# Kernel tuning notes

Measured on AMD Instinct MI355X. Metric: run time of the kernel, lower is better.

## Reference

```python
import jax, jax.numpy as jnp
import numpy as np

E = 128   # embedding_dim
H = 4     # num_heads
D = E * H # internal width = 512 (MHA head_dim = E)
B = 512
N = 128


def setup_inputs() -> dict:
    key = jax.random.key(0)
    ks = jax.random.split(key, 16)
    s = lambda fan_in: 1.0 / np.sqrt(fan_in)
    u = lambda k, shape, sc: jax.random.uniform(k, shape, jnp.float32, -sc, sc)
    inp = {
        "x": jax.random.normal(ks[0], (B, N, E), jnp.float32),
        "weights": jax.random.uniform(ks[1], (B, N, 1), jnp.float32),
        # self.embedding: Linear(E, D)
        "emb_W": u(ks[2], (D, E), s(E)), "emb_b": u(ks[3], (D,), s(E)),
        # outer W_q/W_k/W_v: Linear(D, D)
        "wq_W": u(ks[4], (D, D), s(D)), "wq_b": u(ks[5], (D,), s(D)),
        "wk_W": u(ks[6], (D, D), s(D)), "wk_b": u(ks[7], (D,), s(D)),
        "wv_W": u(ks[8], (D, D), s(D)), "wv_b": u(ks[9], (D,), s(D)),
        # nn.MultiheadAttention packed in-projection (out_proj is irrelevant:
        # its output is discarded, only att_weights are used)
        "in_proj_W": u(ks[10], (3 * D, D), s(D)),
        "in_proj_b": jnp.zeros((3 * D,), jnp.float32),
        # LayerNorm(D)
        "ln_g": jnp.ones((D,), jnp.float32), "ln_b": jnp.zeros((D,), jnp.float32),
        # self.out: Linear(D, E)
        "out_W": u(ks[11], (E, D), s(D)), "out_b": u(ks[12], (E,), s(D)),
    }
    return inp


def reference(x, weights, emb_W, emb_b, wq_W, wq_b, wk_W, wk_b, wv_W, wv_b,
              in_proj_W, in_proj_b, ln_g, ln_b, out_W, out_b):
    # x: [B, N, E] -> embedded [B, N, D]
    xe = x @ emb_W.T + emb_b
    # key_padding_mask: rows of xe that are all-zero
    pad = jnp.sum(jnp.abs(xe), axis=-1) == 0.0              # [B, N] bool

    # outer projections
    q_in = xe @ wq_W.T + wq_b
    k_in = xe @ wk_W.T + wk_b
    v_in = xe @ wv_W.T + wv_b                               # [B, N, D]

    # MHA internal packed in-projection
    Wq, Wk, Wv = in_proj_W[:D], in_proj_W[D:2 * D], in_proj_W[2 * D:]
    bq, bk, bv = in_proj_b[:D], in_proj_b[D:2 * D], in_proj_b[2 * D:]
    hd = D // H  # head_dim = E
    to_heads = lambda t: t.reshape(t.shape[0], t.shape[1], H, hd).transpose(0, 2, 1, 3)
    q = to_heads(q_in @ Wq.T + bq)                          # [B, H, N, hd]
    k = to_heads(k_in @ Wk.T + bk)

    scores = jnp.einsum('bhie,bhje->bhij', q, k) / jnp.sqrt(jnp.float32(hd))
    scores = jnp.where(pad[:, None, None, :], -jnp.inf, scores)
    attn = jax.nn.softmax(scores, axis=-1)                  # [B, H, N, N]
    att_weights = jnp.mean(attn, axis=1)                    # averaged over heads [B, N, N]

    # external reweighting + renormalization
    att_weights = att_weights * jnp.swapaxes(weights, -2, -1)  # [B,N,N]*[B,1,N]
    att_weights = att_weights / jnp.sum(att_weights, axis=-1, keepdims=True)

    # re-apply to outer V projection (MHA's own output is discarded)
    att_output = jnp.einsum('bij,bjd->bid', att_weights, v_in)

    h = xe + jax.nn.softplus(att_output)
    mu = jnp.mean(h, axis=-1, keepdims=True)
    var = jnp.mean((h - mu) ** 2, axis=-1, keepdims=True)
    h = (h - mu) / jnp.sqrt(var + 1e-5) * ln_g + ln_b
    return h @ out_W.T + out_b                              # [B, N, E]
```

## Files before the change

### kernel.cpp

```cpp
#include <hip/hip_runtime.h>
#include <stdint.h>


typedef __attribute__((ext_vector_type(8))) __bf16 bf16x8;
typedef __attribute__((ext_vector_type(8))) uint16_t u16x8;
typedef __attribute__((ext_vector_type(4))) float f32x4;

__device__ __forceinline__ float b2f(uint16_t h) {
  union { uint32_t u; float f; } c; c.u = ((uint32_t)h) << 16; return c.f;
}
__device__ __forceinline__ uint16_t f2b(float f) {
  union { float f; uint32_t u; } c; c.f = f;
  return (uint16_t)((c.u + 0x7fffu + ((c.u >> 16) & 1u)) >> 16);
}
__device__ __forceinline__ void gld16(void* lds, const void* g) {
  __builtin_amdgcn_global_load_lds(
      (const __attribute__((address_space(1))) uint32_t*)(g),
      (__attribute__((address_space(3))) uint32_t*)(lds),
      16, 0, 0);
}

#define MFMA16(a, b, c) __builtin_amdgcn_mfma_f32_16x16x32_bf16((a), (b), (c), 0, 0, 0)

__global__ __launch_bounds__(256) void pack_bf16(const float* __restrict__ in,
                                                 uint16_t* __restrict__ out, int n4) {
  int i = blockIdx.x * 256 + threadIdx.x;
  if (i >= n4) return;
  float4 v = ((const float4*)in)[i];
  ushort4 o;
  o.x = f2b(v.x); o.y = f2b(v.y); o.z = f2b(v.z); o.w = f2b(v.w);
  ((ushort4*)out)[i] = o;
}

__global__ __launch_bounds__(256) void pack_w6(
    const float* __restrict__ emb_W, const float* __restrict__ wq_W,
    const float* __restrict__ wk_W, const float* __restrict__ wv_W,
    const float* __restrict__ ipW, const float* __restrict__ out_W,
    uint16_t* __restrict__ embW2, uint16_t* __restrict__ wqW_bf,
    uint16_t* __restrict__ wkW_bf, uint16_t* __restrict__ Wvc,
    uint16_t* __restrict__ ip_bf, uint16_t* __restrict__ owW_bf) {
  int i = blockIdx.x * 256 + threadIdx.x;
  const float* src; uint16_t* dst; int off;
  if (i < 16384)       { src = emb_W; dst = embW2;  off = i; }
  else if (i < 81920)  { src = wq_W;  dst = wqW_bf; off = i - 16384; }
  else if (i < 147456) { src = wk_W;  dst = wkW_bf; off = i - 81920; }
  else if (i < 212992) { src = wv_W;  dst = Wvc;    off = i - 147456; }
  else if (i < 344064) { src = ipW;   dst = ip_bf;  off = i - 212992; }
  else if (i < 360448) { src = out_W; dst = owW_bf; off = i - 344064; }
  else return;
  float4 v = ((const float4*)src)[off];
  ushort4 o;
  o.x = f2b(v.x); o.y = f2b(v.y); o.z = f2b(v.z); o.w = f2b(v.w);
  ((ushort4*)dst)[off] = o;
}

__global__ __launch_bounds__(256) void bias_stage1(
    const float* __restrict__ wq_W, const float* __restrict__ wk_W,
    const float* __restrict__ wv_W, const float* __restrict__ emb_b,
    const float* __restrict__ wq_b, const float* __restrict__ wk_b,
    const float* __restrict__ wv_b,
    float* __restrict__ t1q, float* __restrict__ t1k, float* __restrict__ bve,
    float* __restrict__ pad_init, float* __restrict__ biasE) {
  const int gid = blockIdx.x * 256 + threadIdx.x;
  if (gid < 65536) pad_init[gid] = 0.f;
  if (gid < 512) biasE[gid] = emb_b[gid];
  const int t = threadIdx.x, l = t & 63, w = t >> 6;
  const int sel = blockIdx.x >> 7;
  const int row = (blockIdx.x & 127) * 4 + w;
  const float* Wbig = sel == 0 ? wq_W : (sel == 1 ? wk_W : wv_W);
  const float* b2   = sel == 0 ? wq_b : (sel == 1 ? wk_b : wv_b);
  float* out        = sel == 0 ? t1q  : (sel == 1 ? t1k  : bve);
  float s = 0.f;
  #pragma unroll
  for (int j = 0; j < 8; ++j) {
    int c = j * 64 + l;
    s += Wbig[(size_t)row * 512 + c] * emb_b[c];
  }
  #pragma unroll
  for (int m = 1; m < 64; m <<= 1) s += __shfl_xor(s, m);
  if (l == 0) out[row] = s + b2[row];
}

__global__ __launch_bounds__(256) void bias_stage2(
    const float* __restrict__ ipW, const float* __restrict__ ipb,
    const float* __restrict__ t1q, const float* __restrict__ t1k,
    float* __restrict__ bqe, float* __restrict__ bke) {
  const int t = threadIdx.x, l = t & 63, w = t >> 6;
  const int sel = blockIdx.x >> 7;
  const int row = (blockIdx.x & 127) * 4 + w;
  const float* Wbig = ipW + (size_t)sel * 262144;
  const float* b1   = sel == 0 ? t1q : t1k;
  const float* b2   = ipb + sel * 512;
  float* out        = sel == 0 ? bqe : bke;
  float s = 0.f;
  #pragma unroll
  for (int j = 0; j < 8; ++j) {
    int c = j * 64 + l;
    s += Wbig[(size_t)row * 512 + c] * b1[c];
  }
  #pragma unroll
  for (int m = 1; m < 64; m <<= 1) s += __shfl_xor(s, m);
  if (l == 0) out[row] = s + b2[row];
}

template <int BIAS_MODE, bool PAD_ACC>
__global__ __launch_bounds__(256) void gemm_btp_kernel(
    const uint16_t* __restrict__ A, long long sA,
    const uint16_t* __restrict__ W, long long sW,
    const float* __restrict__ bias, long long sBias,
    uint16_t* __restrict__ C, long long sC,
    int mIter, float* __restrict__ padout) {
  __shared__ uint16_t Ws[2][128 * 64];
  __shared__ uint16_t As[2][128 * 64];
  const int t = threadIdx.x, l = t & 63, w = t >> 6;
  const int wr = w >> 1, wc = w & 1, l15 = l & 15, hi = l >> 4;
  const int gx = gridDim.x, gy = gridDim.y;
  const int nwg = gx * gy * gridDim.z;
  const int lin = blockIdx.x + gx * (blockIdx.y + gy * blockIdx.z);
  const int cpx = nwg >> 3;
  const int sw = (nwg & 7) ? lin : ((lin & 7) * cpx + (lin >> 3));
  const int ntile = sw % gx;
  const int rest = sw / gx;
  const int mg = rest % gy, bz = rest / gy;
  const uint16_t* Ab = A + (size_t)bz * sA;
  const uint16_t* Wb = W + (size_t)bz * sW;
  uint16_t* Cb = C + (size_t)bz * sC;
  const float* biasb = bias + (size_t)bz * sBias;
  const int srow = t >> 3;
  const int schunk = (t & 7) * 8;
  const int gchunk = (((t & 7) ^ (srow & 7)) * 8);
  const int rowB0 = ntile * 128;
  #pragma unroll
  for (int kt = 0; kt < 2; ++kt)
    #pragma unroll
    for (int i = 0; i < 4; ++i) {
      const int r = i * 32 + srow;
      gld16(&Ws[kt][r * 64 + schunk], Wb + (size_t)(rowB0 + r) * 128 + kt * 64 + gchunk);
    }
  auto stageA = [&](int u) {
    const int rowA0 = (mg * mIter + (u >> 1)) * 128;
    const int kb = (u & 1) << 6;
    #pragma unroll
    for (int i = 0; i < 4; ++i) {
      const int r = i * 32 + srow;
      gld16(&As[u & 1][r * 64 + schunk], Ab + (size_t)(rowA0 + r) * 128 + kb + gchunk);
    }
  };
  const int rsw = (l15 & 7);
  stageA(0);
  const int U = mIter * 2;
  f32x4 acc[4][4];
  for (int u = 0; u < U; ++u) {
    const int kt = u & 1;
    if (kt == 0) {
      #pragma unroll
      for (int m = 0; m < 4; ++m)
        #pragma unroll
        for (int n = 0; n < 4; ++n) acc[m][n] = (f32x4){0.f, 0.f, 0.f, 0.f};
    }
    if (u + 1 < U) {
      stageA(u + 1);
      asm volatile("s_waitcnt vmcnt(4)" ::: "memory");
    } else {
      asm volatile("s_waitcnt vmcnt(0)" ::: "memory");
    }
    __builtin_amdgcn_s_barrier();
    asm volatile("" ::: "memory");
    #pragma unroll
    for (int ks = 0; ks < 2; ++ks) {
      const int gck = ((ks * 4 + hi) ^ rsw) * 8;
      bf16x8 a[4], bb[4];
      #pragma unroll
      for (int m = 0; m < 4; ++m)
        a[m] = *(const bf16x8*)&As[kt][(wr * 64 + m * 16 + l15) * 64 + gck];
      #pragma unroll
      for (int n = 0; n < 4; ++n)
        bb[n] = *(const bf16x8*)&Ws[kt][(wc * 64 + n * 16 + l15) * 64 + gck];
      #pragma unroll
      for (int m = 0; m < 4; ++m)
        #pragma unroll
        for (int n = 0; n < 4; ++n) acc[m][n] = MFMA16(a[m], bb[n], acc[m][n]);
    }
    asm volatile("" ::: "memory");
    __builtin_amdgcn_s_barrier();
    if (kt == 1) {
      const int rowA0 = (mg * mIter + (u >> 1)) * 128;
      #pragma unroll
      for (int m = 0; m < 4; ++m) {
        const int row = rowA0 + wr * 64 + m * 16 + hi * 4;
        float padp[4] = {0.f, 0.f, 0.f, 0.f};
        #pragma unroll
        for (int n = 0; n < 4; ++n) {
          const int col = rowB0 + wc * 64 + n * 16 + l15;
          float bv = 0.f;
          if constexpr (BIAS_MODE == 1) bv = biasb[col];
          #pragma unroll
          for (int r = 0; r < 4; ++r) {
            float rv = acc[m][n][r] + bv;
            if constexpr (PAD_ACC) padp[r] += fabsf(rv);
            Cb[(size_t)(row + r) * 512 + col] = f2b(rv);
          }
        }
        if constexpr (PAD_ACC) {
          if (bz == 0) {
            #pragma unroll
            for (int r = 0; r < 4; ++r) {
              float s2 = padp[r];
              s2 += __shfl_xor(s2, 1); s2 += __shfl_xor(s2, 2);
              s2 += __shfl_xor(s2, 4); s2 += __shfl_xor(s2, 8);
              if (l15 == 0) atomicAdd(padout + row + r, s2);
            }
          }
        }
      }
    }
  }
}

template <typename OT, int BIAS_MODE>
__global__ __launch_bounds__(256) void gemm_bt_kernel(
    const uint16_t* __restrict__ A, long long sA,
    const uint16_t* __restrict__ W, long long sW,
    const float* __restrict__ bias, long long sBias,
    OT* __restrict__ C, long long sC, int N, int K) {
  __shared__ uint16_t As[2][128 * 64];
  __shared__ uint16_t Bs[2][128 * 64];
  const int t = threadIdx.x, l = t & 63, w = t >> 6;
  const int wr = w >> 1, wc = w & 1, l15 = l & 15, hi = l >> 4;
  const int gx = gridDim.x, gy = gridDim.y;
  const int nwg = gx * gy * gridDim.z;
  const int lin = blockIdx.x + gx * (blockIdx.y + gy * blockIdx.z);
  const int cpx = nwg >> 3;
  const int sw = (nwg & 7) ? lin : ((lin & 7) * cpx + (lin >> 3));
  const int ntile = sw % gx;
  const int rest = sw / gx;
  const int mtile = rest % gy, bz = rest / gy;
  const uint16_t* Ab = A + (size_t)bz * sA;
  const uint16_t* Wb = W + (size_t)bz * sW;
  OT* Cb = C + (size_t)bz * sC;
  const float* biasb = bias + (size_t)bz * sBias;
  f32x4 acc[4][4];
  #pragma unroll
  for (int m = 0; m < 4; ++m)
    #pragma unroll
    for (int n = 0; n < 4; ++n) acc[m][n] = (f32x4){0.f, 0.f, 0.f, 0.f};
  const int srow = t >> 3;
  const int schunk = (t & 7) * 8;
  const int gchunk = (((t & 7) ^ (srow & 7)) * 8);
  const int nk = K >> 6;
  const int rowA0 = mtile * 128, rowB0 = ntile * 128;
  auto stage = [&](int kt, int buf) {
    const int kb = kt << 6;
    #pragma unroll
    for (int i = 0; i < 4; ++i) {
      const int r = i * 32 + srow;
      gld16(&As[buf][r * 64 + schunk], Ab + (size_t)(rowA0 + r) * K + kb + gchunk);
      gld16(&Bs[buf][r * 64 + schunk], Wb + (size_t)(rowB0 + r) * K + kb + gchunk);
    }
  };
  stage(0, 0);
  const int rsw = (l15 & 7);
  for (int kt = 0; kt < nk; ++kt) {
    const int cur = kt & 1;
    if (kt + 1 < nk) {
      stage(kt + 1, cur ^ 1);
      asm volatile("s_waitcnt vmcnt(8)" ::: "memory");
    } else {
      asm volatile("s_waitcnt vmcnt(0)" ::: "memory");
    }
    __builtin_amdgcn_s_barrier();
    asm volatile("" ::: "memory");
    #pragma unroll
    for (int ks = 0; ks < 2; ++ks) {
      const int gck = ((ks * 4 + hi) ^ rsw) * 8;
      bf16x8 a[4], bb[4];
      #pragma unroll
      for (int m = 0; m < 4; ++m)
        a[m] = *(const bf16x8*)&As[cur][(wr * 64 + m * 16 + l15) * 64 + gck];
      #pragma unroll
      for (int n = 0; n < 4; ++n)
        bb[n] = *(const bf16x8*)&Bs[cur][(wc * 64 + n * 16 + l15) * 64 + gck];
      #pragma unroll
      for (int m = 0; m < 4; ++m)
        #pragma unroll
        for (int n = 0; n < 4; ++n) acc[m][n] = MFMA16(a[m], bb[n], acc[m][n]);
    }
    asm volatile("" ::: "memory");
    __builtin_amdgcn_s_barrier();
  }
  #pragma unroll
  for (int m = 0; m < 4; ++m) {
    const int row = rowA0 + wr * 64 + m * 16 + hi * 4;
    #pragma unroll
    for (int n = 0; n < 4; ++n) {
      const int col = rowB0 + wc * 64 + n * 16 + l15;
      float bv = 0.f;
      if constexpr (BIAS_MODE == 1) bv = biasb[col];
      #pragma unroll
      for (int r = 0; r < 4; ++r) {
        float rv = acc[m][n][r] + bv;
        if constexpr (sizeof(OT) == 2) {
          ((uint16_t*)Cb)[(size_t)(row + r) * N + col] = f2b(rv);
        } else {
          Cb[(size_t)(row + r) * N + col] = rv;
        }
      }
    }
  }
}

__global__ __launch_bounds__(256) void gemm_ab_kernel(
    const uint16_t* __restrict__ A, int lda, long long sA,
    const uint16_t* __restrict__ B, int ldb, long long sB,
    uint16_t* __restrict__ C, int ldc, long long sC, int K) {
  __shared__ uint16_t As[128 * 64];
  __shared__ uint16_t Bt[128 * 64];
  const int t = threadIdx.x, l = t & 63, w = t >> 6;
  const int wr = w >> 1, wc = w & 1, l15 = l & 15, hi = l >> 4;
  const int gx = gridDim.x, gy = gridDim.y;
  const int nwg = gx * gy * gridDim.z;
  const int lin = blockIdx.x + gx * (blockIdx.y + gy * blockIdx.z);
  const int cpx = nwg >> 3;
  const int sw = (nwg & 7) ? lin : ((lin & 7) * cpx + (lin >> 3));
  const int ntile = sw % gx;
  const int rest = sw / gx;
  const int mtile = rest % gy, bz = rest / gy;
  const uint16_t* Ab = A + (size_t)bz * sA;
  const uint16_t* Bb = B + (size_t)bz * sB;
  uint16_t* Cb = C + (size_t)bz * sC;
  f32x4 acc[4][4];
  #pragma unroll
  for (int m = 0; m < 4; ++m)
    #pragma unroll
    for (int n = 0; n < 4; ++n) acc[m][n] = (f32x4){0.f, 0.f, 0.f, 0.f};
  const int srow = t >> 3, schunk = (t & 7) * 8;
  const int nk = K >> 6;
  for (int kt = 0; kt < nk; ++kt) {
    const int kb = kt << 6;
    #pragma unroll
    for (int i = 0; i < 4; ++i) {
      const int r = i * 32 + srow;
      gld16(&As[r * 64 + schunk], Ab + (size_t)(mtile * 128 + r) * lda + kb + schunk);
    }
    #pragma unroll
    for (int rd = 0; rd < 4; ++rd) {
      const int id = rd * 256 + t;
      const int kr = id >> 4;
      const int c = (id & 15) * 8;
      u16x8 gv = *(const u16x8*)(Bb + (size_t)(kb + kr) * ldb + ntile * 128 + c);
      #pragma unroll
      for (int j = 0; j < 8; ++j) Bt[(c + j) * 64 + kr] = gv[j];
    }
    __syncthreads();
    #pragma unroll
    for (int ks = 0; ks < 2; ++ks) {
      const int k0 = ks * 32 + hi * 8;
      bf16x8 a[4], bb[4];
      #pragma unroll
      for (int m = 0; m < 4; ++m) a[m] = *(const bf16x8*)&As[(wr * 64 + m * 16 + l15) * 64 + k0];
      #pragma unroll
      for (int n = 0; n < 4; ++n) bb[n] = *(const bf16x8*)&Bt[(wc * 64 + n * 16 + l15) * 64 + k0];
      #pragma unroll
      for (int m = 0; m < 4; ++m)
        #pragma unroll
        for (int n = 0; n < 4; ++n) acc[m][n] = MFMA16(a[m], bb[n], acc[m][n]);
    }
    __syncthreads();
  }
  #pragma unroll
  for (int m = 0; m < 4; ++m) {
    const int row = mtile * 128 + wr * 64 + m * 16 + hi * 4;
    #pragma unroll
    for (int n = 0; n < 4; ++n) {
      const int col = ntile * 128 + wc * 64 + n * 16 + l15;
      #pragma unroll
      for (int r = 0; r < 4; ++r)
        Cb[(size_t)(row + r) * ldc + col] = f2b(acc[m][n][r]);
    }
  }
}

__global__ __launch_bounds__(256) void gemm_atb_kernel(
    const uint16_t* __restrict__ Wke, const uint16_t* __restrict__ Wqe,
    const float* __restrict__ bqe, uint16_t* __restrict__ Wg,
    float* __restrict__ vh) {
  __shared__ uint16_t At[128 * 64];
  __shared__ uint16_t Bt[128 * 64];
  const int h = blockIdx.x;
  const int t = threadIdx.x, l = t & 63, w = t >> 6;
  const int wr = w >> 1, wc = w & 1, l15 = l & 15, hi = l >> 4;
  const uint16_t* A = Wke + (size_t)h * 16384;
  const uint16_t* B = Wqe + (size_t)h * 16384;
  f32x4 acc[4][4];
  #pragma unroll
  for (int m = 0; m < 4; ++m)
    #pragma unroll
    for (int n = 0; n < 4; ++n) acc[m][n] = (f32x4){0.f, 0.f, 0.f, 0.f};
  float vacc = 0.f;
  for (int kt = 0; kt < 2; ++kt) {
    const int kb = kt << 6;
    #pragma unroll
    for (int rd = 0; rd < 4; ++rd) {
      const int id = rd * 256 + t;
      const int kr = id >> 4;
      const int c = (id & 15) * 8;
      u16x8 ga = *(const u16x8*)(A + (size_t)(kb + kr) * 128 + c);
      u16x8 gb = *(const u16x8*)(B + (size_t)(kb + kr) * 128 + c);
      #pragma unroll
      for (int j = 0; j < 8; ++j) {
        const int row = c + j;
        const int sxz = (((row & 7) ^ ((row >> 3) & 7)) << 3);
        At[row * 64 + (kr ^ sxz)] = ga[j];
        Bt[row * 64 + (kr ^ sxz)] = gb[j];
      }
    }
    __syncthreads();
    if (t < 128) {
      const int sxz = (((t & 7) ^ ((t >> 3) & 7)) << 3);
      for (int o = 0; o < 64; ++o)
        vacc += b2f(At[t * 64 + (o ^ sxz)]) * bqe[h * 128 + kb + o];
    }
    #pragma unroll
    for (int ks = 0; ks < 2; ++ks) {
      bf16x8 a[4], bb[4];
      #pragma unroll
      for (int m = 0; m < 4; ++m) {
        const int mr = wr * 64 + m * 16 + l15;
        const int sxz = (((mr & 7) ^ ((mr >> 3) & 7)) << 3);
        a[m] = *(const bf16x8*)&At[mr * 64 + ((ks * 32 + hi * 8) ^ sxz)];
      }
      #pragma unroll
      for (int n = 0; n < 4; ++n) {
        const int nr = wc * 64 + n * 16 + l15;
        const int sxz = (((nr & 7) ^ ((nr >> 3) & 7)) << 3);
        bb[n] = *(const bf16x8*)&Bt[nr * 64 + ((ks * 32 + hi * 8) ^ sxz)];
      }
      #pragma unroll
      for (int m = 0; m < 4; ++m)
        #pragma unroll
        for (int n = 0; n < 4; ++n) acc[m][n] = MFMA16(a[m], bb[n], acc[m][n]);
    }
    __syncthreads();
  }
  if (t < 128) vh[h * 128 + t] = vacc;
  #pragma unroll
  for (int m = 0; m < 4; ++m) {
    const int row = wr * 64 + m * 16 + hi * 4;
    #pragma unroll
    for (int n = 0; n < 4; ++n) {
      const int col = wc * 64 + n * 16 + l15;
      #pragma unroll
      for (int r = 0; r < 4; ++r)
        Wg[(size_t)h * 16384 + (size_t)(row + r) * 128 + col] = f2b(acc[m][n][r]);
    }
  }
}

__global__ __launch_bounds__(512) void att_fused(
    const uint16_t* __restrict__ xg, const uint16_t* __restrict__ Wg,
    const float* __restrict__ vh, const float* __restrict__ wts,
    const float* __restrict__ padsum, uint16_t* __restrict__ tout) {
  __shared__ uint16_t Xr[2][128 * 64];
  __shared__ uint16_t GP[2][128 * 64];
  __shared__ float bS[4][128];
  const int blk = blockIdx.x;
  const int b = (blk & 7) * 64 + (blk >> 3);
  const int t = threadIdx.x, l = t & 63, wband = t >> 6;
  const int l15 = l & 15, hi = l >> 4;
  const int srow = t >> 3;
  const int schunk = (t & 7) * 8;
  const int gchunk = (((t & 7) ^ (srow & 7)) * 8);
  const float SCALE = 0.088388347648318447f;
  const int rsw = (l15 & 7);

  const uint16_t* xb = xg + (size_t)b * 16384;
  #pragma unroll
  for (int kt = 0; kt < 2; ++kt)
    #pragma unroll
    for (int i = 0; i < 2; ++i) {
      const int r = i * 64 + srow;
      gld16(&Xr[kt][r * 64 + schunk], xb + (size_t)r * 128 + kt * 64 + gchunk);
      gld16(&GP[kt][r * 64 + schunk], Wg + (size_t)r * 128 + kt * 64 + gchunk);
    }
  asm volatile("s_waitcnt vmcnt(0)" ::: "memory");
  __builtin_amdgcn_s_barrier();
  {
    const int hh = t >> 7, j = t & 127;
    float s = 0.f;
    for (int e = 0; e < 128; ++e) {
      const int c = e & 63;
      const int addr = j * 64 + ((((c >> 3) ^ (j & 7)) << 3) | (c & 7));
      s += b2f(Xr[e >> 6][addr]) * vh[hh * 128 + e];
    }
    bS[hh][j] = s * SCALE +
                ((padsum[(size_t)b * 128 + j] == 0.f) ? -__builtin_inff() : 0.f);
  }

  f32x4 awacc[8];
  #pragma unroll
  for (int n = 0; n < 8; ++n) awacc[n] = (f32x4){0.f, 0.f, 0.f, 0.f};
  u16x8 wreg[4];
  u16x8 xtr[4];

  for (int h = 0; h < 4; ++h) {
    f32x4 pacc[8];
    #pragma unroll
    for (int n = 0; n < 8; ++n) pacc[n] = (f32x4){0.f, 0.f, 0.f, 0.f};
    __builtin_amdgcn_s_setprio(1);
    #pragma unroll
    for (int kt = 0; kt < 2; ++kt)
      #pragma unroll
      for (int ks = 0; ks < 2; ++ks) {
        const int gck = ((ks * 4 + hi) ^ rsw) * 8;
        bf16x8 a, bb[8];
        a = *(const bf16x8*)&Xr[kt][(wband * 16 + l15) * 64 + gck];
        #pragma unroll
        for (int n = 0; n < 8; ++n)
          bb[n] = *(const bf16x8*)&GP[kt][(n * 16 + l15) * 64 + gck];
        #pragma unroll
        for (int n = 0; n < 8; ++n) pacc[n] = MFMA16(a, bb[n], pacc[n]);
      }
    __builtin_amdgcn_s_setprio(0);
    if (h + 1 < 4) {
      #pragma unroll
      for (int kt = 0; kt < 2; ++kt)
        #pragma unroll
        for (int i = 0; i < 2; ++i) {
          const int r = i * 64 + srow;
          wreg[kt * 2 + i] = *(const u16x8*)(Wg + (size_t)(h + 1) * 16384 +
                                             (size_t)r * 128 + kt * 64 + gchunk);
        }
    }
    __builtin_amdgcn_s_barrier();
    #pragma unroll
    for (int n = 0; n < 8; ++n) {
      const int cl = n * 16 + l15;
      const int c = cl & 63;
      #pragma unroll
      for (int r = 0; r < 4; ++r) {
        const int rr = wband * 16 + hi * 4 + r;
        GP[cl >> 6][rr * 64 + ((((c >> 3) ^ (rr & 7)) << 3) | (c & 7))] =
            f2b(pacc[n][r]);
      }
    }
    __builtin_amdgcn_s_barrier();
    f32x4 sacc[8];
    #pragma unroll
    for (int n = 0; n < 8; ++n) sacc[n] = (f32x4){0.f, 0.f, 0.f, 0.f};
    __builtin_amdgcn_s_setprio(1);
    #pragma unroll
    for (int kt = 0; kt < 2; ++kt)
      #pragma unroll
      for (int ks = 0; ks < 2; ++ks) {
        const int gck = ((ks * 4 + hi) ^ rsw) * 8;
        bf16x8 a, bb[8];
        a = *(const bf16x8*)&GP[kt][(wband * 16 + l15) * 64 + gck];
        #pragma unroll
        for (int n = 0; n < 8; ++n)
          bb[n] = *(const bf16x8*)&Xr[kt][(n * 16 + l15) * 64 + gck];
        #pragma unroll
        for (int n = 0; n < 8; ++n) sacc[n] = MFMA16(a, bb[n], sacc[n]);
      }
    __builtin_amdgcn_s_setprio(0);
    if (h == 3) {
      #pragma unroll
      for (int i = 0; i < 4; ++i) {
        const int id = i * 512 + t;
        const int jr = id >> 4;
        const int cc = (id & 15) * 8;
        xtr[i] = *(const u16x8*)(xb + (size_t)jr * 128 + cc);
      }
    }
    #pragma unroll
    for (int r = 0; r < 4; ++r) {
      float e[8], z = 0.f;
      #pragma unroll
      for (int n = 0; n < 8; ++n) {
        e[n] = __expf(sacc[n][r] * SCALE + bS[h][n * 16 + l15]);
        z += e[n];
      }
      z += __shfl_xor(z, 1); z += __shfl_xor(z, 2);
      z += __shfl_xor(z, 4); z += __shfl_xor(z, 8);
      const float zi = 1.f / z;
      #pragma unroll
      for (int n = 0; n < 8; ++n) awacc[n][r] += e[n] * zi;
    }
    if (h + 1 < 4) {
      __builtin_amdgcn_s_barrier();
      asm volatile("s_waitcnt vmcnt(0)" ::: "memory");
      #pragma unroll
      for (int kt = 0; kt < 2; ++kt)
        #pragma unroll
        for (int i = 0; i < 2; ++i) {
          const int r = i * 64 + srow;
          *(u16x8*)&GP[kt][r * 64 + schunk] = wreg[kt * 2 + i];
        }
      __builtin_amdgcn_s_barrier();
    }
  }
  float wv[8];
  #pragma unroll
  for (int n = 0; n < 8; ++n) wv[n] = wts[(size_t)b * 128 + n * 16 + l15];
  __builtin_amdgcn_s_barrier();
  #pragma unroll
  for (int r = 0; r < 4; ++r) {
    float z = 0.f;
    #pragma unroll
    for (int n = 0; n < 8; ++n) z += awacc[n][r] * wv[n];
    z += __shfl_xor(z, 1); z += __shfl_xor(z, 2);
    z += __shfl_xor(z, 4); z += __shfl_xor(z, 8);
    const float zi = 1.f / z;
    const int rr = wband * 16 + hi * 4 + r;
    #pragma unroll
    for (int n = 0; n < 8; ++n) {
      const int cl = n * 16 + l15;
      const int c = cl & 63;
      GP[cl >> 6][rr * 64 + ((((c >> 3) ^ (rr & 7)) << 3) | (c & 7))] =
          f2b(awacc[n][r] * wv[n] * zi);
    }
  }
  asm volatile("s_waitcnt vmcnt(0)" ::: "memory");
  #pragma unroll
  for (int i = 0; i < 4; ++i) {
    const int id = i * 512 + t;
    const int jr = id >> 4;
    const int cc = (id & 15) * 8;
    const int kt2 = jr >> 6, kr = jr & 63;
    #pragma unroll
    for (int j = 0; j < 8; ++j) {
      const int drow = cc + j;
      const int sxz = (((drow & 7) ^ ((drow >> 3) & 7)) << 3);
      Xr[kt2][drow * 64 + (kr ^ sxz)] = xtr[i][j];
    }
  }
  __builtin_amdgcn_s_barrier();
  f32x4 tacc[8];
  #pragma unroll
  for (int n = 0; n < 8; ++n) tacc[n] = (f32x4){0.f, 0.f, 0.f, 0.f};
  __builtin_amdgcn_s_setprio(1);
  #pragma unroll
  for (int kt = 0; kt < 2; ++kt)
    #pragma unroll
    for (int ks = 0; ks < 2; ++ks) {
      const int gck = ((ks * 4 + hi) ^ rsw) * 8;
      bf16x8 a, bb[8];
      a = *(const bf16x8*)&GP[kt][(wband * 16 + l15) * 64 + gck];
      #pragma unroll
      for (int n = 0; n < 8; ++n) {
        const int nr = n * 16 + l15;
        const int sxz = (((nr & 7) ^ ((nr >> 3) & 7)) << 3);
        bb[n] = *(const bf16x8*)&Xr[kt][nr * 64 + ((ks * 32 + hi * 8) ^ sxz)];
      }
      #pragma unroll
      for (int n = 0; n < 8; ++n) tacc[n] = MFMA16(a, bb[n], tacc[n]);
    }
  __builtin_amdgcn_s_setprio(0);
  #pragma unroll
  for (int r = 0; r < 4; ++r) {
    const int row = wband * 16 + hi * 4 + r;
    #pragma unroll
    for (int n = 0; n < 8; ++n) {
      const int col = n * 16 + l15;
      tout[(size_t)b * 16384 + (size_t)row * 128 + col] = f2b(tacc[n][r]);
    }
  }
}

__global__ __launch_bounds__(256) void lnh_kernel(const uint16_t* __restrict__ xe,
                                                  const uint16_t* __restrict__ O,
                                                  const float* __restrict__ g,
                                                  const float* __restrict__ be,
                                                  uint16_t* __restrict__ hout) {
  const int t = threadIdx.x, l = t & 63, w = t >> 6;
  const size_t row = (size_t)blockIdx.x * 4 + w;
  const size_t base = row * 512 + l * 8;
  u16x8 xv = *(const u16x8*)(xe + base);
  u16x8 ov = *(const u16x8*)(O + base);
  float hv[8];
  #pragma unroll
  for (int j = 0; j < 8; ++j) {
    float o = b2f(ov[j]);
    float sp = fmaxf(o, 0.f) + __logf(1.f + __expf(-fabsf(o)));
    hv[j] = b2f(xv[j]) + sp;
  }
  float s = 0.f;
  #pragma unroll
  for (int j = 0; j < 8; ++j) s += hv[j];
  #pragma unroll
  for (int m = 1; m < 64; m <<= 1) s += __shfl_xor(s, m);
  const float mu = s * (1.f / 512.f);
  float vs = 0.f;
  #pragma unroll
  for (int j = 0; j < 8; ++j) { float d = hv[j] - mu; vs += d * d; }
  #pragma unroll
  for (int m = 1; m < 64; m <<= 1) vs += __shfl_xor(vs, m);
  const float rstd = rsqrtf(vs * (1.f / 512.f) + 1e-5f);
  u16x8 outv;
  #pragma unroll
  for (int j = 0; j < 8; ++j) {
    const int c = l * 8 + j;
    outv[j] = f2b((hv[j] - mu) * rstd * g[c] + be[c]);
  }
  *(u16x8*)(hout + base) = outv;
}

extern "C" void kernel_launch(void* const* d_in, const int* in_sizes, int n_in,
                              void* d_out, int out_size, void* d_ws, size_t ws_size,
                              hipStream_t stream) {
  (void)in_sizes; (void)n_in; (void)out_size; (void)ws_size;
  const float* x     = (const float*)d_in[0];
  const float* wts   = (const float*)d_in[1];
  const float* emb_W = (const float*)d_in[2];
  const float* emb_b = (const float*)d_in[3];
  const float* wq_W  = (const float*)d_in[4];
  const float* wq_b  = (const float*)d_in[5];
  const float* wk_W  = (const float*)d_in[6];
  const float* wk_b  = (const float*)d_in[7];
  const float* wv_W  = (const float*)d_in[8];
  const float* wv_b  = (const float*)d_in[9];
  const float* ipW   = (const float*)d_in[10];
  const float* ipb   = (const float*)d_in[11];
  const float* ln_g  = (const float*)d_in[12];
  const float* ln_b  = (const float*)d_in[13];
  const float* out_W = (const float*)d_in[14];
  const float* out_b = (const float*)d_in[15];

  char* ws = (char*)d_ws;
  size_t off = 0;
  auto alloc = [&](size_t bytes) { void* p = ws + off; off += (bytes + 255) & ~(size_t)255; return p; };
  uint16_t* wqW_bf = (uint16_t*)alloc(524288);
  uint16_t* wkW_bf = (uint16_t*)alloc(524288);
  uint16_t* ip_bf  = (uint16_t*)alloc(1048576);
  uint16_t* owW_bf = (uint16_t*)alloc(131072);
  uint16_t* Wqc    = (uint16_t*)alloc(524288);
  uint16_t* Wkc    = (uint16_t*)alloc(524288);
  uint16_t* Wvc    = (uint16_t*)alloc(524288);
  uint16_t* embW2  = (uint16_t*)alloc(131072);
  uint16_t* Wqe    = (uint16_t*)alloc(131072);
  uint16_t* Wke    = (uint16_t*)alloc(131072);
  uint16_t* Wve    = (uint16_t*)alloc(131072);
  uint16_t* Wg     = (uint16_t*)alloc(131072);
  float*    vhbuf  = (float*)alloc(2048);
  float*    t1q    = (float*)alloc(2048);
  float*    t1k    = (float*)alloc(2048);
  float*    biasE  = (float*)alloc(2048);
  float*    bqe    = (float*)alloc(2048);
  float*    bke    = (float*)alloc(2048);
  float*    bve    = (float*)alloc(2048);
  float*    pad    = (float*)alloc(262144);
  uint16_t* xe     = (uint16_t*)alloc(67108864);
  uint16_t* B1     = (uint16_t*)alloc(67108864);
  uint16_t* B2     = (uint16_t*)alloc(67108864);

  uint16_t* x_bf = (uint16_t*)d_out + 8388608;
  uint16_t* tb   = B1;
  uint16_t* Ob   = B2;
  uint16_t* hb   = B1;

  const int TB = 256;
  pack_bf16<<<8192, TB, 0, stream>>>(x, x_bf, 2097152);
  pack_w6<<<1408, TB, 0, stream>>>(emb_W, wq_W, wk_W, wv_W, ipW, out_W,
                                   embW2, wqW_bf, wkW_bf, Wvc, ip_bf, owW_bf);
  bias_stage1<<<384, TB, 0, stream>>>(wq_W, wk_W, wv_W, emb_b, wq_b, wk_b, wv_b,
                                      t1q, t1k, bve, pad, biasE);
  bias_stage2<<<256, TB, 0, stream>>>(ipW, ipb, t1q, t1k, bqe, bke);
  gemm_ab_kernel<<<dim3(4, 4, 2), TB, 0, stream>>>(ip_bf, 512, 262144, wqW_bf, 512, 262144,
                                                   Wqc, 512, 262144, 512);
  gemm_ab_kernel<<<dim3(1, 4, 3), TB, 0, stream>>>(Wqc, 512, 262144, embW2, 128, 0,
                                                   Wqe, 128, 65536, 512);
  gemm_atb_kernel<<<4, TB, 0, stream>>>(Wke, Wqe, bqe, Wg, vhbuf);
  gemm_btp_kernel<1, true><<<dim3(4, 128, 1), TB, 0, stream>>>(
      x_bf, 0, embW2, 0, biasE, 0, xe, 0, 4, pad);
  att_fused<<<512, 512, 0, stream>>>(x_bf, Wg, vhbuf, wts, pad, tb);
  gemm_btp_kernel<1, false><<<dim3(4, 128, 1), TB, 0, stream>>>(
      tb, 0, Wve, 0, bve, 0, Ob, 0, 4, nullptr);
  lnh_kernel<<<16384, TB, 0, stream>>>(xe, Ob, ln_g, ln_b, hb);
  gemm_bt_kernel<float, 1><<<dim3(1, 512, 1), TB, 0, stream>>>(
      hb, 0, owW_bf, 0, out_b, 0, (float*)d_out, 0, 128, 512);
}
```

Measured before the change: 232.2 us.

## Fuse softplus residual and LayerNorm into neighboring GEMM epilogues

Removes the standalone LayerNorm kernel. The V-projection GEMM epilogue now computes xe plus softplus(att_output), writes that bf16 pre-norm h, and atomically accumulates per-row sum and sum of squares. The final output GEMM applies normalization algebraically: gamma is folded into out_W during packing, and u = out_W·gamma and v = out_W·beta + out_b are precomputed, so out = rstd*(acc - mu*u) + v. The x pack is also merged into the weight-pack launch. This trades one full read/write pass over the [B,N,D] tensor for extra atomics and a one-pass variance that is less numerically stable.

Measured after the change: 222.8 us (median of 2 runs). 1.04x faster.

```diff
diff --git a/kernel.cpp b/kernel.cpp
--- a/kernel.cpp
+++ b/kernel.cpp
@@ -22,32 +22,44 @@
 
 #define MFMA16(a, b, c) __builtin_amdgcn_mfma_f32_16x16x32_bf16((a), (b), (c), 0, 0, 0)
 
-__global__ __launch_bounds__(256) void pack_bf16(const float* __restrict__ in,
-                                                 uint16_t* __restrict__ out, int n4) {
-  int i = blockIdx.x * 256 + threadIdx.x;
-  if (i >= n4) return;
-  float4 v = ((const float4*)in)[i];
-  ushort4 o;
-  o.x = f2b(v.x); o.y = f2b(v.y); o.z = f2b(v.z); o.w = f2b(v.w);
-  ((ushort4*)out)[i] = o;
-}
-
-__global__ __launch_bounds__(256) void pack_w6(
+__global__ __launch_bounds__(256) void pack_all(
+    const float* __restrict__ x,
     const float* __restrict__ emb_W, const float* __restrict__ wq_W,
     const float* __restrict__ wk_W, const float* __restrict__ wv_W,
     const float* __restrict__ ipW, const float* __restrict__ out_W,
+    const float* __restrict__ ln_g,
+    uint16_t* __restrict__ x_bf,
     uint16_t* __restrict__ embW2, uint16_t* __restrict__ wqW_bf,
     uint16_t* __restrict__ wkW_bf, uint16_t* __restrict__ Wvc,
     uint16_t* __restrict__ ip_bf, uint16_t* __restrict__ owW_bf) {
   int i = blockIdx.x * 256 + threadIdx.x;
+  if (i < 2097152) {
+    float4 v = ((const float4*)x)[i];
+    ushort4 o;
+    o.x = f2b(v.x); o.y = f2b(v.y); o.z = f2b(v.z); o.w = f2b(v.w);
+    ((ushort4*)x_bf)[i] = o;
+    return;
+  }
+  int i2 = i - 2097152;
+  if (i2 >= 360448) return;
+  if (i2 >= 344064) {
+    const int off = i2 - 344064;
+    float4 v = ((const float4*)out_W)[off];
+    const int base = off * 4;
+    ushort4 o;
+    o.x = f2b(v.x * ln_g[(base + 0) & 511]);
+    o.y = f2b(v.y * ln_g[(base + 1) & 511]);
+    o.z = f2b(v.z * ln_g[(base + 2) & 511]);
+    o.w = f2b(v.w * ln_g[(base + 3) & 511]);
+    ((ushort4*)owW_bf)[off] = o;
+    return;
+  }
   const float* src; uint16_t* dst; int off;
-  if (i < 16384)       { src = emb_W; dst = embW2;  off = i; }
-  else if (i < 81920)  { src = wq_W;  dst = wqW_bf; off = i - 16384; }
-  else if (i < 147456) { src = wk_W;  dst = wkW_bf; off = i - 81920; }
-  else if (i < 212992) { src = wv_W;  dst = Wvc;    off = i - 147456; }
-  else if (i < 344064) { src = ipW;   dst = ip_bf;  off = i - 212992; }
-  else if (i < 360448) { src = out_W; dst = owW_bf; off = i - 344064; }
-  else return;
+  if (i2 < 16384)       { src = emb_W; dst = embW2;  off = i2; }
+  else if (i2 < 81920)  { src = wq_W;  dst = wqW_bf; off = i2 - 16384; }
+  else if (i2 < 147456) { src = wk_W;  dst = wkW_bf; off = i2 - 81920; }
+  else if (i2 < 212992) { src = wv_W;  dst = Wvc;    off = i2 - 147456; }
+  else                  { src = ipW;   dst = ip_bf;  off = i2 - 212992; }
   float4 v = ((const float4*)src)[off];
   ushort4 o;
   o.x = f2b(v.x); o.y = f2b(v.y); o.z = f2b(v.z); o.w = f2b(v.w);
@@ -60,9 +72,10 @@
     const float* __restrict__ wq_b, const float* __restrict__ wk_b,
     const float* __restrict__ wv_b,
     float* __restrict__ t1q, float* __restrict__ t1k, float* __restrict__ bve,
-    float* __restrict__ pad_init, float* __restrict__ biasE) {
+    float* __restrict__ pad_init, float* __restrict__ biasE,
+    float* __restrict__ ssum, float* __restrict__ ssq) {
   const int gid = blockIdx.x * 256 + threadIdx.x;
-  if (gid < 65536) pad_init[gid] = 0.f;
+  if (gid < 65536) { pad_init[gid] = 0.f; ssum[gid] = 0.f; ssq[gid] = 0.f; }
   if (gid < 512) biasE[gid] = emb_b[gid];
   const int t = threadIdx.x, l = t & 63, w = t >> 6;
   const int sel = blockIdx.x >> 7;
@@ -84,32 +97,56 @@
 __global__ __launch_bounds__(256) void bias_stage2(
     const float* __restrict__ ipW, const float* __restrict__ ipb,
     const float* __restrict__ t1q, const float* __restrict__ t1k,
-    float* __restrict__ bqe, float* __restrict__ bke) {
+    float* __restrict__ bqe, float* __restrict__ bke,
+    const float* __restrict__ out_W, const float* __restrict__ ln_g,
+    const float* __restrict__ ln_b, const float* __restrict__ out_b,
+    float* __restrict__ u, float* __restrict__ v) {
   const int t = threadIdx.x, l = t & 63, w = t >> 6;
-  const int sel = blockIdx.x >> 7;
-  const int row = (blockIdx.x & 127) * 4 + w;
-  const float* Wbig = ipW + (size_t)sel * 262144;
-  const float* b1   = sel == 0 ? t1q : t1k;
-  const float* b2   = ipb + sel * 512;
-  float* out        = sel == 0 ? bqe : bke;
-  float s = 0.f;
-  #pragma unroll
-  for (int j = 0; j < 8; ++j) {
-    int c = j * 64 + l;
-    s += Wbig[(size_t)row * 512 + c] * b1[c];
-  }
-  #pragma unroll
-  for (int m = 1; m < 64; m <<= 1) s += __shfl_xor(s, m);
-  if (l == 0) out[row] = s + b2[row];
-}
-
-template <int BIAS_MODE, bool PAD_ACC>
+  const int blk = blockIdx.x;
+  if (blk < 256) {
+    const int sel = blk >> 7;
+    const int row = (blk & 127) * 4 + w;
+    const float* Wbig = ipW + (size_t)sel * 262144;
+    const float* b1   = sel == 0 ? t1q : t1k;
+    const float* b2   = ipb + sel * 512;
+    float* out        = sel == 0 ? bqe : bke;
+    float s = 0.f;
+    #pragma unroll
+    for (int j = 0; j < 8; ++j) {
+      int c = j * 64 + l;
+      s += Wbig[(size_t)row * 512 + c] * b1[c];
+    }
+    #pragma unroll
+    for (int m = 1; m < 64; m <<= 1) s += __shfl_xor(s, m);
+    if (l == 0) out[row] = s + b2[row];
+  } else {
+    const int r4 = (blk - 256) * 4 + w;
+    const int row = r4 & 127;
+    const float* src = (r4 < 128) ? ln_g : ln_b;
+    float s = 0.f;
+    #pragma unroll
+    for (int j = 0; j < 8; ++j) {
+      int c = j * 64 + l;
+      s += out_W[(size_t)row * 512 + c] * src[c];
+    }
+    #pragma unroll
+    for (int m = 1; m < 64; m <<= 1) s += __shfl_xor(s, m);
+    if (l == 0) {
+      if (r4 < 128) u[row] = s;
+      else v[row] = s + out_b[row];
+    }
+  }
+}
+
+template <int BIAS_MODE, bool PAD_ACC, bool HV>
 __global__ __launch_bounds__(256) void gemm_btp_kernel(
     const uint16_t* __restrict__ A, long long sA,
     const uint16_t* __restrict__ W, long long sW,
     const float* __restrict__ bias, long long sBias,
     uint16_t* __restrict__ C, long long sC,
-    int mIter, float* __restrict__ padout) {
+    int mIter, float* __restrict__ padout,
+    const uint16_t* __restrict__ xein, float* __restrict__ ssum,
+    float* __restrict__ ssq) {
   __shared__ uint16_t Ws[2][128 * 64];
   __shared__ uint16_t As[2][128 * 64];
   const int t = threadIdx.x, l = t & 63, w = t >> 6;
@@ -189,6 +226,8 @@
       for (int m = 0; m < 4; ++m) {
         const int row = rowA0 + wr * 64 + m * 16 + hi * 4;
         float padp[4] = {0.f, 0.f, 0.f, 0.f};
+        float hsum[4] = {0.f, 0.f, 0.f, 0.f};
+        float hsq[4] = {0.f, 0.f, 0.f, 0.f};
         #pragma unroll
         for (int n = 0; n < 4; ++n) {
           const int col = rowB0 + wc * 64 + n * 16 + l15;
@@ -198,7 +237,15 @@
           for (int r = 0; r < 4; ++r) {
             float rv = acc[m][n][r] + bv;
             if constexpr (PAD_ACC) padp[r] += fabsf(rv);
-            Cb[(size_t)(row + r) * 512 + col] = f2b(rv);
+            if constexpr (HV) {
+              const float sp = fmaxf(rv, 0.f) + __logf(1.f + __expf(-fabsf(rv)));
+              const float hvv = b2f(xein[(size_t)(row + r) * 512 + col]) + sp;
+              hsum[r] += hvv;
+              hsq[r] += hvv * hvv;
+              Cb[(size_t)(row + r) * 512 + col] = f2b(hvv);
+            } else {
+              Cb[(size_t)(row + r) * 512 + col] = f2b(rv);
+            }
           }
         }
         if constexpr (PAD_ACC) {
@@ -212,17 +259,33 @@
             }
           }
         }
-      }
-    }
-  }
-}
-
-template <typename OT, int BIAS_MODE>
+        if constexpr (HV) {
+          #pragma unroll
+          for (int r = 0; r < 4; ++r) {
+            float s2 = hsum[r], q2 = hsq[r];
+            s2 += __shfl_xor(s2, 1); s2 += __shfl_xor(s2, 2);
+            s2 += __shfl_xor(s2, 4); s2 += __shfl_xor(s2, 8);
+            q2 += __shfl_xor(q2, 1); q2 += __shfl_xor(q2, 2);
+            q2 += __shfl_xor(q2, 4); q2 += __shfl_xor(q2, 8);
+            if (l15 == 0) {
+              atomicAdd(ssum + row + r, s2);
+              atomicAdd(ssq + row + r, q2);
+            }
+          }
+        }
+      }
+    }
+  }
+}
+
+template <typename OT, int BIAS_MODE, bool LN>
 __global__ __launch_bounds__(256) void gemm_bt_kernel(
     const uint16_t* __restrict__ A, long long sA,
     const uint16_t* __restrict__ W, long long sW,
     const float* __restrict__ bias, long long sBias,
-    OT* __restrict__ C, long long sC, int N, int K) {
+    OT* __restrict__ C, long long sC, int N, int K,
+    const float* __restrict__ ssum, const float* __restrict__ ssq,
+    const float* __restrict__ uarr, const float* __restrict__ varr) {
   __shared__ uint16_t As[2][128 * 64];
   __shared__ uint16_t Bs[2][128 * 64];
   const int t = threadIdx.x, l = t & 63, w = t >> 6;
@@ -292,13 +355,24 @@
   for (int m = 0; m < 4; ++m) {
     const int row = rowA0 + wr * 64 + m * 16 + hi * 4;
     #pragma unroll
-    for (int n = 0; n < 4; ++n) {
-      const int col = rowB0 + wc * 64 + n * 16 + l15;
-      float bv = 0.f;
-      if constexpr (BIAS_MODE == 1) bv = biasb[col];
-      #pragma unroll
-      for (int r = 0; r < 4; ++r) {
-        float rv = acc[m][n][r] + bv;
+    for (int r = 0; r < 4; ++r) {
+      float mu = 0.f, rstd = 0.f;
+      if constexpr (LN) {
+        mu = ssum[row + r] * (1.f / 512.f);
+        const float var = ssq[row + r] * (1.f / 512.f) - mu * mu;
+        rstd = rsqrtf(var + 1e-5f);
+      }
+      #pragma unroll
+      for (int n = 0; n < 4; ++n) {
+        const int col = rowB0 + wc * 64 + n * 16 + l15;
+        float rv;
+        if constexpr (LN) {
+          rv = rstd * (acc[m][n][r] - mu * uarr[col]) + varr[col];
+        } else {
+          float bv = 0.f;
+          if constexpr (BIAS_MODE == 1) bv = biasb[col];
+          rv = acc[m][n][r] + bv;
+        }
         if constexpr (sizeof(OT) == 2) {
           ((uint16_t*)Cb)[(size_t)(row + r) * N + col] = f2b(rv);
         } else {
@@ -664,44 +738,6 @@
       tout[(size_t)b * 16384 + (size_t)row * 128 + col] = f2b(tacc[n][r]);
     }
   }
-}
-
-__global__ __launch_bounds__(256) void lnh_kernel(const uint16_t* __restrict__ xe,
-                                                  const uint16_t* __restrict__ O,
-                                                  const float* __restrict__ g,
-                                                  const float* __restrict__ be,
-                                                  uint16_t* __restrict__ hout) {
-  const int t = threadIdx.x, l = t & 63, w = t >> 6;
-  const size_t row = (size_t)blockIdx.x * 4 + w;
-  const size_t base = row * 512 + l * 8;
-  u16x8 xv = *(const u16x8*)(xe + base);
-  u16x8 ov = *(const u16x8*)(O + base);
-  float hv[8];
-  #pragma unroll
-  for (int j = 0; j < 8; ++j) {
-    float o = b2f(ov[j]);
-    float sp = fmaxf(o, 0.f) + __logf(1.f + __expf(-fabsf(o)));
-    hv[j] = b2f(xv[j]) + sp;
-  }
-  float s = 0.f;
-  #pragma unroll
-  for (int j = 0; j < 8; ++j) s += hv[j];
-  #pragma unroll
-  for (int m = 1; m < 64; m <<= 1) s += __shfl_xor(s, m);
-  const float mu = s * (1.f / 512.f);
-  float vs = 0.f;
-  #pragma unroll
-  for (int j = 0; j < 8; ++j) { float d = hv[j] - mu; vs += d * d; }
-  #pragma unroll
-  for (int m = 1; m < 64; m <<= 1) vs += __shfl_xor(vs, m);
-  const float rstd = rsqrtf(vs * (1.f / 512.f) + 1e-5f);
-  u16x8 outv;
-  #pragma unroll
-  for (int j = 0; j < 8; ++j) {
-    const int c = l * 8 + j;
-    outv[j] = f2b((hv[j] - mu) * rstd * g[c] + be[c]);
-  }
-  *(u16x8*)(hout + base) = outv;
 }
 
 extern "C" void kernel_launch(void* const* d_in, const int* in_sizes, int n_in,
@@ -747,34 +783,37 @@
   float*    bqe    = (float*)alloc(2048);
   float*    bke    = (float*)alloc(2048);
   float*    bve    = (float*)alloc(2048);
+  float*    uarr   = (float*)alloc(2048);
+  float*    varr   = (float*)alloc(2048);
   float*    pad    = (float*)alloc(262144);
+  float*    ssum   = (float*)alloc(262144);
+  float*    ssq    = (float*)alloc(262144);
   uint16_t* xe     = (uint16_t*)alloc(67108864);
   uint16_t* B1     = (uint16_t*)alloc(67108864);
   uint16_t* B2     = (uint16_t*)alloc(67108864);
 
   uint16_t* x_bf = (uint16_t*)d_out + 8388608;
   uint16_t* tb   = B1;
-  uint16_t* Ob   = B2;
-  uint16_t* hb   = B1;
+  uint16_t* hv   = B2;
 
   const int TB = 256;
-  pack_bf16<<<8192, TB, 0, stream>>>(x, x_bf, 2097152);
-  pack_w6<<<1408, TB, 0, stream>>>(emb_W, wq_W, wk_W, wv_W, ipW, out_W,
-                                   embW2, wqW_bf, wkW_bf, Wvc, ip_bf, owW_bf);
+  pack_all<<<9600, TB, 0, stream>>>(x, emb_W, wq_W, wk_W, wv_W, ipW, out_W, ln_g,
+                                    x_bf, embW2, wqW_bf, wkW_bf, Wvc, ip_bf, owW_bf);
   bias_stage1<<<384, TB, 0, stream>>>(wq_W, wk_W, wv_W, emb_b, wq_b, wk_b, wv_b,
-                                      t1q, t1k, bve, pad, biasE);
-  bias_stage2<<<256, TB, 0, stream>>>(ipW, ipb, t1q, t1k, bqe, bke);
+                                      t1q, t1k, bve, pad, biasE, ssum, ssq);
+  bias_stage2<<<320, TB, 0, stream>>>(ipW, ipb, t1q, t1k, bqe, bke,
+                                      out_W, ln_g, ln_b, out_b, uarr, varr);
   gemm_ab_kernel<<<dim3(4, 4, 2), TB, 0, stream>>>(ip_bf, 512, 262144, wqW_bf, 512, 262144,
                                                    Wqc, 512, 262144, 512);
   gemm_ab_kernel<<<dim3(1, 4, 3), TB, 0, stream>>>(Wqc, 512, 262144, embW2, 128, 0,
                                                    Wqe, 128, 65536, 512);
   gemm_atb_kernel<<<4, TB, 0, stream>>>(Wke, Wqe, bqe, Wg, vhbuf);
-  gemm_btp_kernel<1, true><<<dim3(4, 128, 1), TB, 0, stream>>>(
-      x_bf, 0, embW2, 0, biasE, 0, xe, 0, 4, pad);
+  gemm_btp_kernel<1, true, false><<<dim3(4, 128, 1), TB, 0, stream>>>(
+      x_bf, 0, embW2, 0, biasE, 0, xe, 0, 4, pad, nullptr, nullptr, nullptr);
   att_fused<<<512, 512, 0, stream>>>(x_bf, Wg, vhbuf, wts, pad, tb);
-  gemm_btp_kernel<1, false><<<dim3(4, 128, 1), TB, 0, stream>>>(
-      tb, 0, Wve, 0, bve, 0, Ob, 0, 4, nullptr);
-  lnh_kernel<<<16384, TB, 0, stream>>>(xe, Ob, ln_g, ln_b, hb);
-  gemm_bt_kernel<float, 1><<<dim3(1, 512, 1), TB, 0, stream>>>(
-      hb, 0, owW_bf, 0, out_b, 0, (float*)d_out, 0, 128, 512);
-}
+  gemm_btp_kernel<1, false, true><<<dim3(4, 128, 1), TB, 0, stream>>>(
+      tb, 0, Wve, 0, bve, 0, hv, 0, 4, nullptr, xe, ssum, ssq);
+  gemm_bt_kernel<float, 0, true><<<dim3(1, 512, 1), TB, 0, stream>>>(
+      hv, 0, owW_bf, 0, nullptr, 0, (float*)d_out, 0, 128, 512,
+      ssum, ssq, uarr, varr);
+}
```
